# Kernel tuning notes

Hardware: AMD Instinct MI355X
Metric: run time of the kernel (lower is better)

Reference implementation:

```python
import jax, jax.numpy as jnp
import numpy as np

N, D, F, M, K = 4096, 1024, 4096, 2048, 307
EPS = 1e-5

def _ln(h, g, b):
    mu = jnp.mean(h, axis=-1, keepdims=True)
    var = jnp.mean(jnp.square(h - mu), axis=-1, keepdims=True)
    return (h - mu) * jax.lax.rsqrt(var + EPS) * g + b

def _attn(h, wq, wk, wv, mask):
    # wq/wk/wv stored as [D, D] so y = h @ w matches torch Linear(h) with W.T
    q = h @ wq
    k = h @ wk
    v = h @ wv
    s = (q @ k.T) * (1.0 / np.sqrt(D))  # [N, N]
    s = jnp.where(mask, -1e9, s)
    a = jax.nn.softmax(s, axis=-1)
    return a @ v, a

def _ffn(h, w1, b1, w2, b2):
    return jax.nn.gelu(h @ w1 + b1, approximate=False) @ w2 + b2

def setup_inputs() -> dict:
    ks = jax.random.split(jax.random.key(0), 32)
    s = 0.02
    p = lambda i, shape: (jax.random.normal(ks[i], shape, jnp.float32) * s)
    inp = {
        'x': jax.random.normal(ks[0], (N, D), jnp.float32),
        'real_edge_mask': jax.random.bernoulli(ks[1], 0.5, (N, N)),
        'fake_edge_mask': jax.random.bernoulli(ks[2], 0.5, (N, N)),
        'mask_nodes': jax.random.permutation(ks[3], N)[:M].astype(jnp.int32),
        'gene_idx': jnp.argsort(jax.random.uniform(ks[4], (M, D)), axis=-1)[:, :K].astype(jnp.int32),
        'wq1': p(5, (D, D)), 'wk1': p(6, (D, D)), 'wv1': p(7, (D, D)),
        'g1': jnp.ones((D,)), 'be1': jnp.zeros((D,)),
        'fw1': p(8, (D, F)), 'fb1': jnp.zeros((F,)),
        'fw2': p(9, (F, D)), 'fb2': jnp.zeros((D,)),
        'g2': jnp.ones((D,)), 'be2': jnp.zeros((D,)),
        'wq2': p(10, (D, D)), 'wk2': p(11, (D, D)), 'wv2': p(12, (D, D)),
        'g3': jnp.ones((D,)), 'be3': jnp.zeros((D,)),
        'hw1': p(13, (D, F)), 'hb1': jnp.zeros((F,)),
        'hw2': p(14, (F, D)), 'hb2': jnp.zeros((D,)),
        'g4': jnp.ones((D,)), 'be4': jnp.zeros((D,)),
        'head_w': p(15, (D, D)), 'head_b': jnp.zeros((D,)),
    }
    return inp

def reference(x, real_edge_mask, fake_edge_mask, mask_nodes, gene_idx,
              wq1, wk1, wv1, g1, be1, fw1, fb1, fw2, fb2, g2, be2,
              wq2, wk2, wv2, g3, be3, hw1, hb1, hw2, hb2, g4, be4,
              head_w, head_b):
    rows = jnp.arange(M)[:, None]  # [M, 1]
    # encoding_mask_nodes: zero K genes in each of M masked cells
    mask_x = x[mask_nodes].at[rows, gene_idx].set(0.0)
    use_x = x.at[mask_nodes].set(mask_x)

    hidden, encode_weights = _attn(use_x, wq1, wk1, wv1, real_edge_mask)
    hidden = _ln(hidden + use_x, g1, be1)
    hidden = _ln(hidden + _ffn(hidden, fw1, fb1, fw2, fb2), g2, be2)
    # NOTE: original `hidden[mask_nodes][gene_mask] = 0` is a no-op (copy), reproduced.

    recon, _decode_weights = _attn(hidden, wq2, wk2, wv2, real_edge_mask)
    recon = _ln(recon + hidden, g3, be3)
    recon = _ln(recon + _ffn(recon, hw1, hb1, hw2, hb2), g4, be4)
    h = recon @ head_w + head_b

    x_init = x[mask_nodes][rows, gene_idx]   # [M, K]
    x_recon = h[mask_nodes][rows, gene_idx]  # [M, K]
    return x_init, x_recon, encode_weights, recon
```

## Files before the change

kernel.cpp:

```cpp
#include <hip/hip_runtime.h>
#include <math.h>
#include <stdint.h>

typedef unsigned short u16;
typedef __attribute__((ext_vector_type(8))) short bf16x8;
typedef __attribute__((ext_vector_type(4))) float f32x4;
typedef __attribute__((ext_vector_type(4))) unsigned short u16x4;

#define N_ 4096
#define D_ 1024
#define F_ 4096
#define M_ 2048
#define KG 307

__device__ __forceinline__ u16 f2bf(float f) {
  unsigned int u = __float_as_uint(f);
  unsigned int r = u + 0x7fffu + ((u >> 16) & 1u);
  return (u16)(r >> 16);
}

__device__ __forceinline__ float bf2f(u16 u) {
  return __uint_as_float((unsigned)u << 16);
}

__device__ __forceinline__ float gelu_fast(float t) {
  float x = t * 0.70710678118654752f;
  float ax = fabsf(x);
  float u = __builtin_amdgcn_rcpf(fmaf(0.3275911f, ax, 1.0f));
  float poly =
      u * fmaf(u, fmaf(u, fmaf(u, fmaf(u, 1.061405429f, -1.453152027f), 1.421413741f),
                       -0.284496736f),
               0.254829592f);
  float erfabs = fmaf(-poly, __expf(-ax * ax), 1.0f);
  float er = copysignf(erfabs, x);
  return 0.5f * t * (1.0f + er);
}

__device__ __forceinline__ void gl_lds16(const u16* g, u16* l) {
  __builtin_amdgcn_global_load_lds(
      (__attribute__((address_space(1))) void*)(void*)g,
      (__attribute__((address_space(3))) void*)(void*)l,
      16, 0, 0);
}

enum { E_QKV = 0, E_SMASK = 1, E_PART = 2, E_GELU = 3 };
#define SMEM_BYTES 131072

template <int EPI, int TN = 256>
__global__ __launch_bounds__(512, 2) void gemm256(
    const u16* __restrict__ A, const u16* __restrict__ B,
    void* __restrict__ C, void* __restrict__ C2,
    int gridM, int gridN, int Ndim, int Ksp, int lda, int ldb, long zstr,
    const float* __restrict__ bias, const unsigned char* __restrict__ mask,
    float scale) {
  constexpr int NV = TN / 64;
  constexpr int WCOLS = TN / 4;
  constexpr int NBCH = TN / 64;
  constexpr int BBYTES = TN * 128;
  extern __shared__ __align__(16) char smem[];
  const int tid = threadIdx.x;
  const int lane = tid & 63;
  const int wid = tid >> 6;
  const int wr = wid >> 2;
  const int wc = wid & 3;
  const int lr = lane & 15;
  const int lk = lane >> 4;

  const int nwg = gridM * gridN;
  const int bid = blockIdx.x;
  const int q8 = nwg >> 3, r8 = nwg & 7;
  const int xcd = bid & 7, ii = bid >> 3;
  int wg = (xcd < r8 ? xcd * (q8 + 1) : r8 * (q8 + 1) + (xcd - r8) * q8) + ii;
  const int rowblk = wg / (gridN << 2);
  const int rem = wg - rowblk * (gridN << 2);
  const int mrem = gridM - (rowblk << 2);
  int mtile, ntile;
  if (mrem >= 4) {
    ntile = rem >> 2;
    mtile = (rowblk << 2) + (rem & 3);
  } else {
    ntile = rem / mrem;
    mtile = (rowblk << 2) + (rem - ntile * mrem);
  }
  const long bm = (long)mtile * 256;
  const long bn = (long)ntile * TN;
  const long koff = (long)blockIdx.y * Ksp;
  const int NT = Ksp >> 6;

  auto stA = [&](int t, int h) {
    char* base = smem + ((t & 1) << 15) + (h << 14);
    const long k0 = koff + ((long)t << 6);
#pragma unroll
    for (int j = 0; j < 2; ++j) {
      int o = tid + (j << 9);
      int r = o >> 3, s = o & 7;
      gl_lds16(A + (bm + (h << 7) + r) * (long)lda + k0 + ((s ^ (r & 7)) << 3),
               (u16*)(base + o * 16));
    }
  };
  auto stB = [&](int t, int c) {
    char* base = smem + 65536 + (t & 1) * BBYTES + (c << 13);
    const long k0 = koff + ((long)t << 6);
    int o = tid;
    int r = o >> 3, s = o & 7;
    gl_lds16(B + (bn + (c << 6) + r) * (long)ldb + k0 + ((s ^ (r & 7)) << 3),
             (u16*)(base + o * 16));
  };

  bf16x8 avA[2][2], avB[2][2], bv[NV][2];
  f32x4 acc[8][NV];
#pragma unroll
  for (int m = 0; m < 8; ++m)
#pragma unroll
    for (int n = 0; n < NV; ++n) acc[m][n] = f32x4{0.f, 0.f, 0.f, 0.f};

  auto rdAV = [&](bf16x8(&av)[2][2], const char* Ab_, int q) {
#pragma unroll
    for (int e = 0; e < 2; ++e)
#pragma unroll
      for (int ks = 0; ks < 2; ++ks) {
        int r = (wr << 7) + (q << 5) + (e << 4) + lr;
        av[e][ks] = *(const bf16x8*)(Ab_ + r * 128 + ((((ks << 2) | lk) ^ (r & 7)) << 4));
      }
  };
  auto rdBV = [&](const char* Bb_) {
#pragma unroll
    for (int n = 0; n < NV; ++n)
#pragma unroll
      for (int ks = 0; ks < 2; ++ks) {
        int r = wc * WCOLS + (n << 4) + lr;
        bv[n][ks] = *(const bf16x8*)(Bb_ + r * 128 + ((((ks << 2) | lk) ^ (r & 7)) << 4));
      }
  };

#define MM(Q, AV)                                                              \
  __builtin_amdgcn_s_setprio(1);                                               \
  _Pragma("unroll") for (int e = 0; e < 2; ++e)                                \
  _Pragma("unroll") for (int n = 0; n < NV; ++n)                               \
  _Pragma("unroll") for (int ks = 0; ks < 2; ++ks)                             \
      acc[((Q) << 1) | e][n] = __builtin_amdgcn_mfma_f32_16x16x32_bf16(        \
          AV[e][ks], bv[n][ks], acc[((Q) << 1) | e][n], 0, 0, 0);              \
  __builtin_amdgcn_s_setprio(0);                                               \
  __builtin_amdgcn_sched_barrier(0);

  stA(0, 0);
  stA(0, 1);
#pragma unroll
  for (int c = 0; c < NBCH; ++c) stB(0, c);
  if (NT > 1) {
#pragma unroll
    for (int c = 0; c < NBCH; ++c) stB(1, c);
    __builtin_amdgcn_sched_barrier(0);
    asm volatile("s_waitcnt vmcnt(%0)" ::"i"(NBCH));
  } else {
    __builtin_amdgcn_sched_barrier(0);
    asm volatile("s_waitcnt vmcnt(0)");
  }
  __builtin_amdgcn_sched_barrier(0);
  __builtin_amdgcn_s_barrier();
  rdAV(avA, smem, 0);
  __builtin_amdgcn_sched_barrier(0);

  for (int t = 0; t < NT; ++t) {
    const char* Ab = smem + ((t & 1) << 15);
    const char* AbN = smem + (((t + 1) & 1) << 15);
    const char* Bb = smem + 65536 + (t & 1) * BBYTES;
    rdBV(Bb);
    rdAV(avB, Ab, 1);
    if (t + 1 < NT) stA(t + 1, 0);
    __builtin_amdgcn_sched_barrier(0);
    asm volatile("s_waitcnt lgkmcnt(4)");
    __builtin_amdgcn_sched_barrier(0);
    MM(0, avA)
    rdAV(avA, Ab, 2);
    if (t + 1 < NT) stA(t + 1, 1);
    __builtin_amdgcn_sched_barrier(0);
    asm volatile("s_waitcnt lgkmcnt(4)");
    __builtin_amdgcn_sched_barrier(0);
    MM(1, avB)
    __builtin_amdgcn_s_barrier();
    rdAV(avB, Ab, 3);
    if (t + 2 < NT) {
      stB(t + 2, 0);
      stB(t + 2, 1);
    }
    __builtin_amdgcn_sched_barrier(0);
    asm volatile("s_waitcnt lgkmcnt(4)");
    __builtin_amdgcn_sched_barrier(0);
    MM(2, avA)
    asm volatile("s_waitcnt lgkmcnt(0)");
    if (t + 2 < NT)
      asm volatile("s_waitcnt vmcnt(2)");
    else
      asm volatile("s_waitcnt vmcnt(0)");
    __builtin_amdgcn_sched_barrier(0);
    __builtin_amdgcn_s_barrier();
    if (t + 1 < NT) rdAV(avA, AbN, 0);
    if (t + 2 < NT) {
#pragma unroll
      for (int c = 2; c < NBCH; ++c) stB(t + 2, c);
    }
    __builtin_amdgcn_sched_barrier(0);
    MM(3, avB)
  }
#undef MM

  const bool z0 = (blockIdx.y == 0);
#pragma unroll
  for (int m = 0; m < 8; ++m) {
#pragma unroll
    for (int n = 0; n < NV; ++n) {
#pragma unroll
      for (int j = 0; j < 4; ++j) {
        long row = bm + (wr << 7) + (m << 4) + (lk << 2) + j;
        long col = bn + wc * WCOLS + (n << 4) + lr;
        float v = acc[m][n][j];
        if constexpr (EPI == E_QKV) {
          if (col < 2048)
            ((u16*)C)[row * 2048 + col] = f2bf(v);
          else
            ((u16*)C2)[(col - 2048) * (long)N_ + row] = f2bf(v);
        } else if constexpr (EPI == E_SMASK) {
          v *= scale;
          if (mask[row * Ndim + col]) v = -1e9f;
          ((u16*)C)[row * Ndim + col] = f2bf(v);
        } else if constexpr (EPI == E_PART) {
          ((u16*)C)[(long)blockIdx.y * zstr + row * Ndim + col] =
              f2bf(v + ((z0 && bias) ? bias[col] : 0.f));
        } else if constexpr (EPI == E_GELU) {
          ((u16*)C)[row * Ndim + col] = f2bf(gelu_fast(v + bias[col]));
        }
      }
    }
  }
}

__global__ __launch_bounds__(256) void gemm_nt_bias(
    const u16* __restrict__ A, const u16* __restrict__ B, float* __restrict__ C,
    int Ndim, int K, int lda, int ldb, const float* __restrict__ bias) {
  __shared__ u16 As[2][128 * 32];
  __shared__ u16 Bs[2][128 * 32];
  const int tid = threadIdx.x;
  const int lane = tid & 63;
  const int wid = tid >> 6;
  const int wr = wid >> 1;
  const int wc = wid & 1;
  const int lr = lane & 15;
  const int lk = lane >> 4;
  const long bm = (long)blockIdx.x * 128;
  const long bn = (long)blockIdx.y * 128;

  f32x4 acc[4][4];
#pragma unroll
  for (int i = 0; i < 4; ++i)
#pragma unroll
    for (int j = 0; j < 4; ++j) acc[i][j] = f32x4{0.f, 0.f, 0.f, 0.f};

  auto stage = [&](int buf, long k0) {
#pragma unroll
    for (int i = 0; i < 2; ++i) {
      int c = tid + i * 256;
      gl_lds16(A + (bm + (c >> 2)) * (long)lda + k0 + (c & 3) * 8, As[buf] + c * 8);
    }
#pragma unroll
    for (int i = 0; i < 2; ++i) {
      int c = tid + i * 256;
      gl_lds16(B + (bn + (c >> 2)) * (long)ldb + k0 + (c & 3) * 8, Bs[buf] + c * 8);
    }
  };

  stage(0, 0);
  __syncthreads();
  const int nt = K / 32;
  int cur = 0;
  for (int t = 0; t < nt; ++t) {
    if (t + 1 < nt) stage(cur ^ 1, (long)(t + 1) * 32);
    bf16x8 av[4], bv[4];
#pragma unroll
    for (int mr = 0; mr < 4; ++mr)
      av[mr] = *(const bf16x8*)(As[cur] + (wr * 64 + mr * 16 + lr) * 32 + lk * 8);
#pragma unroll
    for (int nr = 0; nr < 4; ++nr)
      bv[nr] = *(const bf16x8*)(Bs[cur] + (wc * 64 + nr * 16 + lr) * 32 + lk * 8);
#pragma unroll
    for (int mr = 0; mr < 4; ++mr)
#pragma unroll
      for (int nr = 0; nr < 4; ++nr)
        acc[mr][nr] = __builtin_amdgcn_mfma_f32_16x16x32_bf16(av[mr], bv[nr], acc[mr][nr], 0, 0, 0);
    __syncthreads();
    cur ^= 1;
  }
#pragma unroll
  for (int mr = 0; mr < 4; ++mr)
#pragma unroll
    for (int nr = 0; nr < 4; ++nr)
#pragma unroll
      for (int j = 0; j < 4; ++j) {
        long row = bm + wr * 64 + mr * 16 + lk * 4 + j;
        long col = bn + wc * 64 + nr * 16 + lr;
        C[row * Ndim + col] = acc[mr][nr][j] + bias[col];
      }
}

__global__ __launch_bounds__(256) void tcvt3(const float* __restrict__ in0,
                                             const float* __restrict__ in1,
                                             const float* __restrict__ in2,
                                             u16* __restrict__ out, int R, int C) {
  __shared__ float tile[32][33];
  const float* in = (blockIdx.z == 0) ? in0 : (blockIdx.z == 1 ? in1 : in2);
  u16* dst = out + (size_t)blockIdx.z * R * C;
  int bx = blockIdx.x * 32;
  int by = blockIdx.y * 32;
  int tx = threadIdx.x & 31;
  int ty = threadIdx.x >> 5;
#pragma unroll
  for (int i = 0; i < 32; i += 8)
    tile[ty + i][tx] = in[(long)(by + ty + i) * C + bx + tx];
  __syncthreads();
#pragma unroll
  for (int i = 0; i < 32; i += 8)
    dst[(long)(bx + ty + i) * R + by + tx] = f2bf(tile[tx][ty + i]);
}

__global__ void copy_usex(const float* __restrict__ x, float* __restrict__ xf,
                          u16* __restrict__ xb, long n) {
  long i = (long)blockIdx.x * blockDim.x + threadIdx.x;
  if (i < n) {
    float v = x[i];
    xf[i] = v;
    xb[i] = f2bf(v);
  }
}

__global__ void mask_zero(const float* __restrict__ x, const int* __restrict__ mask_nodes,
                          const int* __restrict__ gene_idx, float* __restrict__ xf,
                          u16* __restrict__ xb, float* __restrict__ x_init) {
  int m = blockIdx.x;
  int k = threadIdx.x;
  if (k >= KG) return;
  int row = mask_nodes[m];
  int col = gene_idx[m * KG + k];
  x_init[m * KG + k] = x[(long)row * D_ + col];
  xf[(long)row * D_ + col] = 0.f;
  xb[(long)row * D_ + col] = 0;
}

template <int NY>
__global__ __launch_bounds__(256) void add_ln(const u16* __restrict__ y, long ystr,
                                              const float* __restrict__ r,
                                              const float* __restrict__ g,
                                              const float* __restrict__ b,
                                              float* __restrict__ of, u16* __restrict__ ob) {
  int row = blockIdx.x;
  const int gi = threadIdx.x * 4;
  const long base = (long)row * D_ + gi;
  f32x4 rv = *(const f32x4*)(r + base);
  u16x4 yv[NY];
#pragma unroll
  for (int z = 0; z < NY; ++z) yv[z] = *(const u16x4*)(y + z * ystr + base);
  float v[4];
  float s = 0.f, ss = 0.f;
#pragma unroll
  for (int i = 0; i < 4; ++i) {
    float t = rv[i];
#pragma unroll
    for (int z = 0; z < NY; ++z) t += bf2f(yv[z][i]);
    v[i] = t;
    s += t;
    ss += t * t;
  }
#pragma unroll
  for (int o = 32; o > 0; o >>= 1) {
    s += __shfl_down(s, o, 64);
    ss += __shfl_down(ss, o, 64);
  }
  __shared__ float red[8];
  int wid = threadIdx.x >> 6, lane = threadIdx.x & 63;
  if (lane == 0) {
    red[wid] = s;
    red[4 + wid] = ss;
  }
  __syncthreads();
  if (threadIdx.x == 0) {
    red[0] = red[0] + red[1] + red[2] + red[3];
    red[4] = red[4] + red[5] + red[6] + red[7];
  }
  __syncthreads();
  float mu = red[0] * (1.f / D_);
  float var = red[4] * (1.f / D_) - mu * mu;
  float rs = rsqrtf(var + 1e-5f);
  f32x4 gv = *(const f32x4*)(g + gi);
  f32x4 bv = *(const f32x4*)(b + gi);
  f32x4 ov;
  u16x4 obv;
#pragma unroll
  for (int i = 0; i < 4; ++i) {
    float o = (v[i] - mu) * rs * gv[i] + bv[i];
    ov[i] = o;
    obv[i] = f2bf(o);
  }
  *(f32x4*)(of + base) = ov;
  *(u16x4*)(ob + base) = obv;
}

template <bool WF32>
__global__ __launch_bounds__(256) void softmax_row(const u16* __restrict__ sin,
                                                   float* __restrict__ a32,
                                                   u16* __restrict__ a16) {
  int row = blockIdx.x;
  const long base = (long)row * N_ + threadIdx.x * 16;
  const u16* sr = sin + base;
  float v[16];
  bf16x8 h0 = *(const bf16x8*)(sr);
  bf16x8 h1 = *(const bf16x8*)(sr + 8);
#pragma unroll
  for (int j = 0; j < 8; ++j) {
    v[j] = bf2f((u16)h0[j]);
    v[8 + j] = bf2f((u16)h1[j]);
  }
  float mx = v[0];
#pragma unroll
  for (int i = 1; i < 16; ++i) mx = fmaxf(mx, v[i]);
#pragma unroll
  for (int o = 32; o > 0; o >>= 1) mx = fmaxf(mx, __shfl_down(mx, o, 64));
  __shared__ float red[8];
  int wid = threadIdx.x >> 6, lane = threadIdx.x & 63;
  if (lane == 0) red[wid] = mx;
  __syncthreads();
  if (threadIdx.x == 0) red[0] = fmaxf(fmaxf(red[0], red[1]), fmaxf(red[2], red[3]));
  __syncthreads();
  mx = red[0];
  float sum = 0.f;
#pragma unroll
  for (int i = 0; i < 16; ++i) {
    v[i] = __expf(v[i] - mx);
    sum += v[i];
  }
#pragma unroll
  for (int o = 32; o > 0; o >>= 1) sum += __shfl_down(sum, o, 64);
  if (lane == 0) red[4 + wid] = sum;
  __syncthreads();
  if (threadIdx.x == 0) red[4] = red[4] + red[5] + red[6] + red[7];
  __syncthreads();
  float inv = 1.f / red[4];
  bf16x8 o0, o1;
#pragma unroll
  for (int j = 0; j < 8; ++j) {
    float p0 = v[j] * inv, p1 = v[8 + j] * inv;
    o0[j] = (short)f2bf(p0);
    o1[j] = (short)f2bf(p1);
    if constexpr (WF32) {
      a32[base + j] = p0;
      a32[base + 8 + j] = p1;
    }
  }
  *(bf16x8*)(a16 + base) = o0;
  *(bf16x8*)(a16 + base + 8) = o1;
}

__global__ void gather_rows(const u16* __restrict__ src, const int* __restrict__ mask_nodes,
                            u16* __restrict__ dst) {
  int m = blockIdx.x;
  int row = mask_nodes[m];
  for (int i = threadIdx.x; i < D_; i += 256)
    dst[(long)m * D_ + i] = src[(long)row * D_ + i];
}

__global__ void gather_recon(const float* __restrict__ h, const int* __restrict__ gene_idx,
                             float* __restrict__ xr) {
  int m = blockIdx.x;
  int k = threadIdx.x;
  if (k >= KG) return;
  xr[m * KG + k] = h[(long)m * D_ + gene_idx[m * KG + k]];
}

extern "C" void kernel_launch(void* const* d_in, const int* in_sizes, int n_in,
                              void* d_out, int out_size, void* d_ws, size_t ws_size,
                              hipStream_t stream) {
  const float* x = (const float*)d_in[0];
  const unsigned char* real_mask = (const unsigned char*)d_in[1];
  const int* mask_nodes = (const int*)d_in[3];
  const int* gene_idx = (const int*)d_in[4];
  const float* wq1 = (const float*)d_in[5];
  const float* wk1 = (const float*)d_in[6];
  const float* wv1 = (const float*)d_in[7];
  const float* g1 = (const float*)d_in[8];
  const float* be1 = (const float*)d_in[9];
  const float* fw1 = (const float*)d_in[10];
  const float* fb1 = (const float*)d_in[11];
  const float* fw2 = (const float*)d_in[12];
  const float* fb2 = (const float*)d_in[13];
  const float* g2 = (const float*)d_in[14];
  const float* be2 = (const float*)d_in[15];
  const float* wq2 = (const float*)d_in[16];
  const float* wk2 = (const float*)d_in[17];
  const float* wv2 = (const float*)d_in[18];
  const float* g3 = (const float*)d_in[19];
  const float* be3 = (const float*)d_in[20];
  const float* hw1 = (const float*)d_in[21];
  const float* hb1 = (const float*)d_in[22];
  const float* hw2 = (const float*)d_in[23];
  const float* hb2 = (const float*)d_in[24];
  const float* g4 = (const float*)d_in[25];
  const float* be4 = (const float*)d_in[26];
  const float* head_w = (const float*)d_in[27];
  const float* head_b = (const float*)d_in[28];

  float* out_xinit = (float*)d_out;
  float* out_xrecon = out_xinit + (long)M_ * KG;
  float* out_enc = out_xrecon + (long)M_ * KG;
  float* out_recon = out_enc + (long)N_ * N_;

  hipFuncSetAttribute((const void*)gemm256<E_QKV, 192>, hipFuncAttributeMaxDynamicSharedMemorySize, SMEM_BYTES);
  hipFuncSetAttribute((const void*)gemm256<E_SMASK>, hipFuncAttributeMaxDynamicSharedMemorySize, SMEM_BYTES);
  hipFuncSetAttribute((const void*)gemm256<E_PART>, hipFuncAttributeMaxDynamicSharedMemorySize, SMEM_BYTES);
  hipFuncSetAttribute((const void*)gemm256<E_GELU>, hipFuncAttributeMaxDynamicSharedMemorySize, SMEM_BYTES);

  char* w = (char*)d_ws;
  size_t off = 0;
  auto alloc = [&](size_t bytes) {
    void* p = w + off;
    off += (bytes + 255) & ~(size_t)255;
    return p;
  };
  float* useXf = (float*)alloc((size_t)N_ * D_ * 4);
  u16* useXb = (u16*)alloc((size_t)N_ * D_ * 2);
  u16* wslot = (u16*)alloc((size_t)D_ * F_ * 2);
  u16* qkb = (u16*)alloc((size_t)N_ * 2048 * 2);
  u16* vT = (u16*)alloc((size_t)D_ * N_ * 2);
  u16* tbuf = (u16*)alloc((size_t)N_ * F_ * 2);
  u16* aB = (u16*)alloc((size_t)N_ * N_ * 2);
  u16* gout4b = (u16*)alloc((size_t)4 * N_ * D_ * 2);
  float* actA = (float*)alloc((size_t)N_ * D_ * 4);
  float* actB = (float*)alloc((size_t)N_ * D_ * 4);
  u16* actB16 = (u16*)alloc((size_t)N_ * D_ * 2);
  u16* AgB = qkb;

  const float scale = 1.0f / 32.0f;
  const long nd = (long)N_ * D_;
  dim3 blk(256), blk5(512);

  copy_usex<<<dim3((unsigned)((nd + 255) / 256)), blk, 0, stream>>>(x, useXf, useXb, nd);
  mask_zero<<<dim3(M_), 320, 0, stream>>>(x, mask_nodes, gene_idx, useXf, useXb, out_xinit);

#define TCVT1(src, R, C, dst) \
  tcvt3<<<dim3((C) / 32, (R) / 32, 1), blk, 0, stream>>>(src, src, src, dst, R, C)
#define TCVTQ(s0, s1, s2, dst) \
  tcvt3<<<dim3(32, 32, 3), blk, 0, stream>>>(s0, s1, s2, dst, 1024, 1024)
#define GQKV(A)                                                                           \
  gemm256<E_QKV, 192><<<dim3(256, 1), blk5, SMEM_BYTES, stream>>>(                        \
      A, wslot, qkb, vT, 16, 16, 3072, 1024, 1024, 1024, 0, nullptr, nullptr, 0.f)
#define G256(EP, GM, GN, Z, A, B, C, C2, ND, KS, LA, LB, ZS, BI, MK, SC)                        \
  gemm256<EP><<<dim3((GM) * (GN), Z), blk5, SMEM_BYTES, stream>>>(A, B, C, C2, GM, GN, ND, KS, \
                                                                  LA, LB, ZS, BI, MK, SC)

  TCVTQ(wq1, wk1, wv1, wslot);
  GQKV(useXb);
  G256(E_SMASK, 16, 16, 1, qkb, qkb + 1024, aB, nullptr, 4096, 1024, 2048, 2048, 0, nullptr, real_mask, scale);
  softmax_row<true><<<dim3(N_), blk, 0, stream>>>(aB, out_enc, aB);
  G256(E_PART, 16, 4, 4, aB, vT, gout4b, nullptr, 1024, 1024, 4096, 4096, nd, nullptr, nullptr, 0.f);
  add_ln<4><<<dim3(N_), blk, 0, stream>>>(gout4b, nd, useXf, g1, be1, actA, actB16);
  TCVT1(fw1, D_, F_, wslot);
  G256(E_GELU, 16, 16, 1, actB16, wslot, tbuf, nullptr, 4096, 1024, 1024, 1024, 0, fb1, nullptr, 0.f);
  TCVT1(fw2, F_, D_, wslot);
  G256(E_PART, 16, 4, 4, tbuf, wslot, gout4b, nullptr, 1024, 1024, 4096, 4096, nd, fb2, nullptr, 0.f);
  add_ln<4><<<dim3(N_), blk, 0, stream>>>(gout4b, nd, actA, g2, be2, actB, actB16);

  TCVTQ(wq2, wk2, wv2, wslot);
  GQKV(actB16);
  G256(E_SMASK, 16, 16, 1, qkb, qkb + 1024, aB, nullptr, 4096, 1024, 2048, 2048, 0, nullptr, real_mask, scale);
  softmax_row<false><<<dim3(N_), blk, 0, stream>>>(aB, nullptr, aB);
  G256(E_PART, 16, 4, 4, aB, vT, gout4b, nullptr, 1024, 1024, 4096, 4096, nd, nullptr, nullptr, 0.f);
  add_ln<4><<<dim3(N_), blk, 0, stream>>>(gout4b, nd, actB, g3, be3, actA, actB16);
  TCVT1(hw1, D_, F_, wslot);
  G256(E_GELU, 16, 16, 1, actB16, wslot, tbuf, nullptr, 4096, 1024, 1024, 1024, 0, hb1, nullptr, 0.f);
  TCVT1(hw2, F_, D_, wslot);
  G256(E_PART, 16, 4, 4, tbuf, wslot, gout4b, nullptr, 1024, 1024, 4096, 4096, nd, hb2, nullptr, 0.f);
  add_ln<4><<<dim3(N_), blk, 0, stream>>>(gout4b, nd, actA, g4, be4, out_recon, actB16);

  gather_rows<<<dim3(M_), blk, 0, stream>>>(actB16, mask_nodes, AgB);
  TCVT1(head_w, D_, D_, wslot);
  gemm_nt_bias<<<dim3(16, 8), blk, 0, stream>>>(AgB, wslot, actA, 1024, 1024, 1024, 1024, head_b);
  gather_recon<<<dim3(M_), 320, 0, stream>>>(actA, gene_idx, out_xrecon);
#undef TCVT1
#undef TCVTQ
#undef GQKV
#undef G256
}
```

Measured before the change: 623.5 us.

## Use bf16 residuals, split-K of two, and drop intermediate fp32 activation writes

Residual inputs to the add+LayerNorm kernels are now read as bf16 instead of fp32, and fp32 activation outputs are written only for the final recon. The split-K partial GEMMs move from four K-splits on a 16x4 tile grid to two K-splits on a 16x8 grid with a 128-wide N tile. This halves the partial-sum buffer traffic and removes the fp32 copies of x and the intermediate activations. The trade-off is extra rounding on the residual path, which may hurt accuracy, and a different GEMM tile shape.

```diff
diff --git a/kernel.cpp b/kernel.cpp
--- a/kernel.cpp
+++ b/kernel.cpp
@@ -322,39 +322,33 @@
     dst[(long)(bx + ty + i) * R + by + tx] = f2bf(tile[tx][ty + i]);
 }
 
-__global__ void copy_usex(const float* __restrict__ x, float* __restrict__ xf,
-                          u16* __restrict__ xb, long n) {
+__global__ void copy_usex(const float* __restrict__ x, u16* __restrict__ xb, long n) {
   long i = (long)blockIdx.x * blockDim.x + threadIdx.x;
-  if (i < n) {
-    float v = x[i];
-    xf[i] = v;
-    xb[i] = f2bf(v);
-  }
+  if (i < n) xb[i] = f2bf(x[i]);
 }
 
 __global__ void mask_zero(const float* __restrict__ x, const int* __restrict__ mask_nodes,
-                          const int* __restrict__ gene_idx, float* __restrict__ xf,
-                          u16* __restrict__ xb, float* __restrict__ x_init) {
+                          const int* __restrict__ gene_idx, u16* __restrict__ xb,
+                          float* __restrict__ x_init) {
   int m = blockIdx.x;
   int k = threadIdx.x;
   if (k >= KG) return;
   int row = mask_nodes[m];
   int col = gene_idx[m * KG + k];
   x_init[m * KG + k] = x[(long)row * D_ + col];
-  xf[(long)row * D_ + col] = 0.f;
   xb[(long)row * D_ + col] = 0;
 }
 
-template <int NY>
+template <int NY, bool WOF>
 __global__ __launch_bounds__(256) void add_ln(const u16* __restrict__ y, long ystr,
-                                              const float* __restrict__ r,
+                                              const u16* __restrict__ r,
                                               const float* __restrict__ g,
                                               const float* __restrict__ b,
                                               float* __restrict__ of, u16* __restrict__ ob) {
   int row = blockIdx.x;
   const int gi = threadIdx.x * 4;
   const long base = (long)row * D_ + gi;
-  f32x4 rv = *(const f32x4*)(r + base);
+  u16x4 rv = *(const u16x4*)(r + base);
   u16x4 yv[NY];
 #pragma unroll
   for (int z = 0; z < NY; ++z) yv[z] = *(const u16x4*)(y + z * ystr + base);
@@ -362,7 +356,7 @@
   float s = 0.f, ss = 0.f;
 #pragma unroll
   for (int i = 0; i < 4; ++i) {
-    float t = rv[i];
+    float t = bf2f(rv[i]);
 #pragma unroll
     for (int z = 0; z < NY; ++z) t += bf2f(yv[z][i]);
     v[i] = t;
@@ -399,7 +393,7 @@
     ov[i] = o;
     obv[i] = f2bf(o);
   }
-  *(f32x4*)(of + base) = ov;
+  if constexpr (WOF) *(f32x4*)(of + base) = ov;
   *(u16x4*)(ob + base) = obv;
 }
 
@@ -513,7 +507,7 @@
 
   hipFuncSetAttribute((const void*)gemm256<E_QKV, 192>, hipFuncAttributeMaxDynamicSharedMemorySize, SMEM_BYTES);
   hipFuncSetAttribute((const void*)gemm256<E_SMASK>, hipFuncAttributeMaxDynamicSharedMemorySize, SMEM_BYTES);
-  hipFuncSetAttribute((const void*)gemm256<E_PART>, hipFuncAttributeMaxDynamicSharedMemorySize, SMEM_BYTES);
+  hipFuncSetAttribute((const void*)gemm256<E_PART, 128>, hipFuncAttributeMaxDynamicSharedMemorySize, SMEM_BYTES);
   hipFuncSetAttribute((const void*)gemm256<E_GELU>, hipFuncAttributeMaxDynamicSharedMemorySize, SMEM_BYTES);
 
   char* w = (char*)d_ws;
@@ -523,25 +517,24 @@
     off += (bytes + 255) & ~(size_t)255;
     return p;
   };
-  float* useXf = (float*)alloc((size_t)N_ * D_ * 4);
   u16* useXb = (u16*)alloc((size_t)N_ * D_ * 2);
   u16* wslot = (u16*)alloc((size_t)D_ * F_ * 2);
   u16* qkb = (u16*)alloc((size_t)N_ * 2048 * 2);
   u16* vT = (u16*)alloc((size_t)D_ * N_ * 2);
   u16* tbuf = (u16*)alloc((size_t)N_ * F_ * 2);
   u16* aB = (u16*)alloc((size_t)N_ * N_ * 2);
-  u16* gout4b = (u16*)alloc((size_t)4 * N_ * D_ * 2);
-  float* actA = (float*)alloc((size_t)N_ * D_ * 4);
-  float* actB = (float*)alloc((size_t)N_ * D_ * 4);
-  u16* actB16 = (u16*)alloc((size_t)N_ * D_ * 2);
+  u16* gout2b = (u16*)alloc((size_t)2 * N_ * D_ * 2);
+  u16* ab1 = (u16*)alloc((size_t)N_ * D_ * 2);
+  u16* ab2 = (u16*)alloc((size_t)N_ * D_ * 2);
   u16* AgB = qkb;
+  float* hout = (float*)gout2b;
 
   const float scale = 1.0f / 32.0f;
   const long nd = (long)N_ * D_;
   dim3 blk(256), blk5(512);
 
-  copy_usex<<<dim3((unsigned)((nd + 255) / 256)), blk, 0, stream>>>(x, useXf, useXb, nd);
-  mask_zero<<<dim3(M_), 320, 0, stream>>>(x, mask_nodes, gene_idx, useXf, useXb, out_xinit);
+  copy_usex<<<dim3((unsigned)((nd + 255) / 256)), blk, 0, stream>>>(x, useXb, nd);
+  mask_zero<<<dim3(M_), 320, 0, stream>>>(x, mask_nodes, gene_idx, useXb, out_xinit);
 
 #define TCVT1(src, R, C, dst) \
   tcvt3<<<dim3((C) / 32, (R) / 32, 1), blk, 0, stream>>>(src, src, src, dst, R, C)
@@ -550,40 +543,44 @@
 #define GQKV(A)                                                                           \
   gemm256<E_QKV, 192><<<dim3(256, 1), blk5, SMEM_BYTES, stream>>>(                        \
       A, wslot, qkb, vT, 16, 16, 3072, 1024, 1024, 1024, 0, nullptr, nullptr, 0.f)
-#define G256(EP, GM, GN, Z, A, B, C, C2, ND, KS, LA, LB, ZS, BI, MK, SC)                        \
-  gemm256<EP><<<dim3((GM) * (GN), Z), blk5, SMEM_BYTES, stream>>>(A, B, C, C2, GM, GN, ND, KS, \
-                                                                  LA, LB, ZS, BI, MK, SC)
+#define GPART(A, B, BI)                                                                   \
+  gemm256<E_PART, 128><<<dim3(128, 2), blk5, SMEM_BYTES, stream>>>(                       \
+      A, B, gout2b, nullptr, 16, 8, 1024, 2048, 4096, 4096, nd, BI, nullptr, 0.f)
+#define G256(EP, GM, GN, A, B, C, ND, KS, LA, LB, BI, MK, SC)                              \
+  gemm256<EP><<<dim3((GM) * (GN), 1), blk5, SMEM_BYTES, stream>>>(                         \
+      A, B, C, nullptr, GM, GN, ND, KS, LA, LB, 0, BI, MK, SC)
 
   TCVTQ(wq1, wk1, wv1, wslot);
   GQKV(useXb);
-  G256(E_SMASK, 16, 16, 1, qkb, qkb + 1024, aB, nullptr, 4096, 1024, 2048, 2048, 0, nullptr, real_mask, scale);
+  G256(E_SMASK, 16, 16, qkb, qkb + 1024, aB, 4096, 1024, 2048, 2048, nullptr, real_mask, scale);
   softmax_row<true><<<dim3(N_), blk, 0, stream>>>(aB, out_enc, aB);
-  G256(E_PART, 16, 4, 4, aB, vT, gout4b, nullptr, 1024, 1024, 4096, 4096, nd, nullptr, nullptr, 0.f);
-  add_ln<4><<<dim3(N_), blk, 0, stream>>>(gout4b, nd, useXf, g1, be1, actA, actB16);
+  GPART(aB, vT, nullptr);
+  add_ln<2, false><<<dim3(N_), blk, 0, stream>>>(gout2b, nd, useXb, g1, be1, nullptr, ab1);
   TCVT1(fw1, D_, F_, wslot);
-  G256(E_GELU, 16, 16, 1, actB16, wslot, tbuf, nullptr, 4096, 1024, 1024, 1024, 0, fb1, nullptr, 0.f);
+  G256(E_GELU, 16, 16, ab1, wslot, tbuf, 4096, 1024, 1024, 1024, fb1, nullptr, 0.f);
   TCVT1(fw2, F_, D_, wslot);
-  G256(E_PART, 16, 4, 4, tbuf, wslot, gout4b, nullptr, 1024, 1024, 4096, 4096, nd, fb2, nullptr, 0.f);
-  add_ln<4><<<dim3(N_), blk, 0, stream>>>(gout4b, nd, actA, g2, be2, actB, actB16);
+  GPART(tbuf, wslot, fb2);
+  add_ln<2, false><<<dim3(N_), blk, 0, stream>>>(gout2b, nd, ab1, g2, be2, nullptr, ab2);
 
   TCVTQ(wq2, wk2, wv2, wslot);
-  GQKV(actB16);
-  G256(E_SMASK, 16, 16, 1, qkb, qkb + 1024, aB, nullptr, 4096, 1024, 2048, 2048, 0, nullptr, real_mask, scale);
+  GQKV(ab2);
+  G256(E_SMASK, 16, 16, qkb, qkb + 1024, aB, 4096, 1024, 2048, 2048, nullptr, real_mask, scale);
   softmax_row<false><<<dim3(N_), blk, 0, stream>>>(aB, nullptr, aB);
-  G256(E_PART, 16, 4, 4, aB, vT, gout4b, nullptr, 1024, 1024, 4096, 4096, nd, nullptr, nullptr, 0.f);
-  add_ln<4><<<dim3(N_), blk, 0, stream>>>(gout4b, nd, actB, g3, be3, actA, actB16);
+  GPART(aB, vT, nullptr);
+  add_ln<2, false><<<dim3(N_), blk, 0, stream>>>(gout2b, nd, ab2, g3, be3, nullptr, ab1);
   TCVT1(hw1, D_, F_, wslot);
-  G256(E_GELU, 16, 16, 1, actB16, wslot, tbuf, nullptr, 4096, 1024, 1024, 1024, 0, hb1, nullptr, 0.f);
+  G256(E_GELU, 16, 16, ab1, wslot, tbuf, 4096, 1024, 1024, 1024, hb1, nullptr, 0.f);
   TCVT1(hw2, F_, D_, wslot);
-  G256(E_PART, 16, 4, 4, tbuf, wslot, gout4b, nullptr, 1024, 1024, 4096, 4096, nd, hb2, nullptr, 0.f);
-  add_ln<4><<<dim3(N_), blk, 0, stream>>>(gout4b, nd, actA, g4, be4, out_recon, actB16);
-
-  gather_rows<<<dim3(M_), blk, 0, stream>>>(actB16, mask_nodes, AgB);
+  GPART(tbuf, wslot, hb2);
+  add_ln<2, true><<<dim3(N_), blk, 0, stream>>>(gout2b, nd, ab1, g4, be4, out_recon, ab2);
+
+  gather_rows<<<dim3(M_), blk, 0, stream>>>(ab2, mask_nodes, AgB);
   TCVT1(head_w, D_, D_, wslot);
-  gemm_nt_bias<<<dim3(16, 8), blk, 0, stream>>>(AgB, wslot, actA, 1024, 1024, 1024, 1024, head_b);
-  gather_recon<<<dim3(M_), 320, 0, stream>>>(actA, gene_idx, out_xrecon);
+  gemm_nt_bias<<<dim3(16, 8), blk, 0, stream>>>(AgB, wslot, hout, 1024, 1024, 1024, 1024, head_b);
+  gather_recon<<<dim3(M_), 320, 0, stream>>>(hout, gene_idx, out_xrecon);
 #undef TCVT1
 #undef TCVTQ
 #undef GQKV
+#undef GPART
 #undef G256
 }
```

Measured after the change: 572.8 us. -8.1%, faster.
